# Optimization experiments

Measured on AMD Instinct MI355X. Metric: run time of the kernel, lower is better.

## Reference

```python
import jax, jax.numpy as jnp
import numpy as np

MARGIN = 0.1
NUM_BINS = 1600  # FastAP histogram bins over squared-distance range [0, 4]


def _fastap_rewards(x, labels):
    """Per-query FastAP (Cakir et al.) with soft (triangular) histogram binning.
    x: [n, d] L2-normalized embeddings; labels: [n] int. Returns [n] rewards.
    Uses the fact that a triangular pulse of width delta spreads each distance
    over exactly two adjacent bins -> scatter-add instead of an [n,n,L] tensor."""
    n = x.shape[0]
    L = NUM_BINS + 1
    delta = 4.0 / NUM_BINS
    dist2 = jnp.clip(2.0 - 2.0 * (x @ x.T), 0.0, 4.0)  # [n, n]
    same = labels[:, None] == labels[None, :]
    eye = jnp.eye(n, dtype=bool)
    i_pos = same & ~eye
    i_neg = ~same

    t = dist2 / delta
    idx0 = jnp.clip(jnp.floor(t).astype(jnp.int32), 0, L - 1)
    idx1 = jnp.clip(idx0 + 1, 0, L - 1)
    frac = t - jnp.floor(t)
    rows = jnp.broadcast_to(jnp.arange(n)[:, None], (n, n))

    def hist(mask):
        m = mask.astype(x.dtype)
        h = jnp.zeros((n, L), x.dtype)
        h = h.at[rows, idx0].add((1.0 - frac) * m)
        h = h.at[rows, idx1].add(frac * m)
        return h

    h_pos = hist(i_pos)
    h_neg = hist(i_neg)
    H_pos = jnp.cumsum(h_pos, axis=1)
    H_all = jnp.cumsum(h_pos + h_neg, axis=1)
    n_pos = jnp.sum(i_pos, axis=1).astype(x.dtype)
    safe = H_all > 0
    ap = jnp.sum(jnp.where(safe, h_pos * H_pos / jnp.where(safe, H_all, 1.0), 0.0), axis=1)
    return jnp.where(n_pos > 0, ap / jnp.maximum(n_pos, 1.0), 0.0)


def _per_row_loss(inputs_col, targets_col, inputs_row, targets_row):
    """Vectorized form of compute_loss_list. Sorting in the original only serves
    to extract max pos / max neg similarity, so per-row maxima + masked sums
    reproduce the exact same math."""
    n = inputs_col.shape[0]
    sim = inputs_col @ inputs_row.T  # [n, m]
    pos = targets_col[:, None] == targets_row[None, :]
    neg = ~pos  # computed BEFORE removing the diagonal, as in the original
    eye = jnp.eye(n, dtype=bool)
    pos = pos.at[:, :n].set(pos[:, :n] & ~eye)

    has_pos = jnp.any(pos, axis=1)
    neg_max = jnp.max(jnp.where(neg, sim, -jnp.inf), axis=1)  # neg_pair_[-1]
    pos_max = jnp.max(jnp.where(pos, sim, -jnp.inf), axis=1)  # pos_pair_[-1]

    pos_sel = pos & (sim < (neg_max + MARGIN)[:, None])
    pos_loss = jnp.sum(jnp.where(pos_sel, 1.0 - sim, 0.0), axis=1)

    thr = jnp.maximum(0.6, pos_max) - MARGIN
    neg_sel = neg & (sim > thr[:, None])
    neg_loss = jnp.sum(jnp.where(neg_sel, sim, 0.0), axis=1)

    return jnp.where(has_pos, pos_loss + neg_loss, 0.0), n


def setup_inputs() -> dict:
    key = jax.random.key(0)
    k1, k2, k3, k4, k5 = jax.random.split(key, 5)
    n, m, d, ncls = 4096, 4096, 128, 512

    def unit(k, shape):
        v = jax.random.normal(k, shape, dtype=jnp.float32)
        return v / jnp.linalg.norm(v, axis=-1, keepdims=True)

    return {
        "inputs_col": unit(k1, (n, d)),
        "targets_col": jax.random.randint(k2, (n,), 0, ncls),
        "inputs_row": unit(k3, (m, d)),
        "targets_row": jax.random.randint(k4, (m,), 0, ncls),
        "reward_labels": jax.random.randint(k5, (n,), 0, ncls),
    }


def reference(inputs_col, targets_col, inputs_row, targets_row, reward_labels):
    loss_i, n = _per_row_loss(inputs_col, targets_col, inputs_row, targets_row)
    # torch.tensor(rewards) detaches rewards from the graph -> stop_gradient
    rewards = jax.lax.stop_gradient(_fastap_rewards(inputs_col, reward_labels))
    return jnp.sum(loss_i * (1.0 - rewards)) / n
```

## Files before the change

kernel.cpp:

```cpp
#include <hip/hip_runtime.h>


#define N_ROWS 4096
#define DIM 128
#define TILE 128
#define L_BINS 1601

typedef __bf16 bf16x8 __attribute__((ext_vector_type(8)));
typedef float f32x4 __attribute__((ext_vector_type(4)));

__device__ __forceinline__ unsigned short f32_to_bf16(float f) {
    unsigned int u = __float_as_uint(f);
    u = (u + 0x7FFFu + ((u >> 16) & 1u)) >> 16;
    return (unsigned short)u;
}

__device__ __forceinline__ float bf16_lo(unsigned int u) {
    return __uint_as_float(u << 16);
}
__device__ __forceinline__ float bf16_hi(unsigned int u) {
    return __uint_as_float(u & 0xFFFF0000u);
}

__device__ __forceinline__ void unpack8(uint4 pk, float* s) {
    s[0] = bf16_lo(pk.x); s[1] = bf16_hi(pk.x);
    s[2] = bf16_lo(pk.y); s[3] = bf16_hi(pk.y);
    s[4] = bf16_lo(pk.z); s[5] = bf16_hi(pk.z);
    s[6] = bf16_lo(pk.w); s[7] = bf16_hi(pk.w);
}

__device__ __forceinline__ void async_copy16(const void* g, void* l) {
    __builtin_amdgcn_global_load_lds(
        (const __attribute__((address_space(1))) unsigned int*)g,
        (__attribute__((address_space(3))) unsigned int*)l, 16, 0, 0);
}

__global__ __launch_bounds__(256) void cvt2_kernel(const float4* __restrict__ a,
                                                   const float4* __restrict__ b,
                                                   ushort4* __restrict__ oa,
                                                   ushort4* __restrict__ ob,
                                                   int nvec) {
    for (int idx = blockIdx.x * 256 + threadIdx.x; idx < 2 * nvec; idx += gridDim.x * 256) {
        bool second = idx >= nvec;
        int k = second ? idx - nvec : idx;
        float4 v = second ? b[k] : a[k];
        ushort4 o;
        o.x = f32_to_bf16(v.x); o.y = f32_to_bf16(v.y);
        o.z = f32_to_bf16(v.z); o.w = f32_to_bf16(v.w);
        if (second) ob[k] = o; else oa[k] = o;
    }
}

__global__ __launch_bounds__(256) void gemm_tile_kernel(const unsigned short* __restrict__ A,
                                                        const unsigned short* __restrict__ B0,
                                                        const unsigned short* __restrict__ B1,
                                                        unsigned short* __restrict__ C0,
                                                        unsigned short* __restrict__ C1,
                                                        int N) {
    __shared__ unsigned short As[TILE * DIM];
    __shared__ unsigned short Bs[TILE * DIM];
    int w = threadIdx.x >> 6;
    int lane = threadIdx.x & 63;
    int tm = blockIdx.y, tn = blockIdx.x;
    const unsigned short* B = blockIdx.z ? B1 : B0;
    unsigned short* C = blockIdx.z ? C1 : C0;

    const char* ga = (const char*)(A + (size_t)tm * TILE * DIM);
    const char* gb = (const char*)(B + (size_t)tn * TILE * DIM);
#pragma unroll
    for (int it = 0; it < 8; ++it) {
        int off = (w * 8 + it) * 1024;
        async_copy16(ga + off + lane * 16, (char*)As + off);
        async_copy16(gb + off + lane * 16, (char*)Bs + off);
    }
    __syncthreads();

    int wm = (w & 1) * 64;
    int wn = (w >> 1) * 64;
    int quad = lane >> 4;
    int l15 = lane & 15;

    f32x4 acc[4][4] = {};
#pragma unroll
    for (int kk = 0; kk < 4; ++kk) {
        int kb = kk * 32 + quad * 8;
        bf16x8 af[4], bfr[4];
#pragma unroll
        for (int mi = 0; mi < 4; ++mi)
            af[mi] = *(const bf16x8*)&As[(wm + mi * 16 + l15) * DIM + kb];
#pragma unroll
        for (int ni = 0; ni < 4; ++ni)
            bfr[ni] = *(const bf16x8*)&Bs[(wn + ni * 16 + l15) * DIM + kb];
#pragma unroll
        for (int mi = 0; mi < 4; ++mi)
#pragma unroll
            for (int ni = 0; ni < 4; ++ni)
                acc[mi][ni] = __builtin_amdgcn_mfma_f32_16x16x32_bf16(af[mi], bfr[ni], acc[mi][ni], 0, 0, 0);
    }

#pragma unroll
    for (int mi = 0; mi < 4; ++mi) {
        int row0 = tm * TILE + wm + mi * 16 + quad * 4;
#pragma unroll
        for (int ni = 0; ni < 4; ++ni) {
            int col = tn * TILE + wn + ni * 16 + l15;
#pragma unroll
            for (int r = 0; r < 4; ++r)
                C[(size_t)(row0 + r) * N + col] = f32_to_bf16(acc[mi][ni][r]);
        }
    }
}

__global__ __launch_bounds__(256) void loss_kernel(const unsigned short* __restrict__ sim,
                                                   const int* __restrict__ tcol,
                                                   const int* __restrict__ trow,
                                                   float* __restrict__ loss,
                                                   int n, int m) {
    int i = (blockIdx.x * 256 + threadIdx.x) >> 6;
    int lane = threadIdx.x & 63;
    int myt = tcol[i];

    const uint4* simv = (const uint4*)(sim + (size_t)i * m);
    const int4* labv = (const int4*)trow;

    uint4 pk[8];
    unsigned long long posm = 0ull, negm = 0ull;
    float pmax = -3e38f, nmax = -3e38f;
#pragma unroll
    for (int v = 0; v < 8; ++v) {
        int vi = v * 64 + lane;
        pk[v] = simv[vi];
        int4 l0 = labv[2 * vi];
        int4 l1 = labv[2 * vi + 1];
        int j0 = vi * 8;
        float s[8];
        unpack8(pk[v], s);
        int lab[8] = {l0.x, l0.y, l0.z, l0.w, l1.x, l1.y, l1.z, l1.w};
#pragma unroll
        for (int k = 0; k < 8; ++k) {
            int j = j0 + k;
            bool same = (lab[k] == myt);
            bool posf = same && (j != i);
            if (posf) pmax = fmaxf(pmax, s[k]);
            if (!same) nmax = fmaxf(nmax, s[k]);
            posm |= ((unsigned long long)posf) << (v * 8 + k);
            negm |= ((unsigned long long)(!same)) << (v * 8 + k);
        }
    }
#pragma unroll
    for (int off = 32; off > 0; off >>= 1) {
        pmax = fmaxf(pmax, __shfl_xor(pmax, off));
        nmax = fmaxf(nmax, __shfl_xor(nmax, off));
    }

    float thr_n = nmax + 0.1f;
    float thr_p = fmaxf(0.6f, pmax) - 0.1f;
    float pl = 0.f, nl = 0.f;
#pragma unroll
    for (int v = 0; v < 8; ++v) {
        float s[8];
        unpack8(pk[v], s);
#pragma unroll
        for (int k = 0; k < 8; ++k) {
            int bit = v * 8 + k;
            bool posf = (posm >> bit) & 1ull;
            bool negf = (negm >> bit) & 1ull;
            pl += (posf && s[k] < thr_n) ? 1.f - s[k] : 0.f;
            nl += (negf && s[k] > thr_p) ? s[k] : 0.f;
        }
    }
    float tot = pl + nl;
#pragma unroll
    for (int off = 32; off > 0; off >>= 1) tot += __shfl_xor(tot, off);
    if (lane == 0) loss[i] = (pmax > -1e30f) ? tot : 0.f;
}

__global__ __launch_bounds__(256) void fastap_kernel(const unsigned short* __restrict__ gram,
                                                     const int* __restrict__ labels,
                                                     float* __restrict__ reward,
                                                     int n) {
    __shared__ unsigned long long hist[L_BINS];
    __shared__ unsigned long long wsum[4];
    __shared__ float apw[4];
    __shared__ int npw[4];
    int i = blockIdx.x;
    int t = threadIdx.x;
    int w = t >> 6;
    int lane = t & 63;

    for (int b = t; b < L_BINS; b += 256) hist[b] = 0ull;
    __syncthreads();

    int li = labels[i];
    int npos = 0;
    const uint4* gv = (const uint4*)(gram + (size_t)i * n);
    const int4* labv = (const int4*)labels;

    for (int v = t; v < (n >> 3); v += 256) {
        uint4 pk = gv[v];
        int4 l0 = labv[2 * v];
        int4 l1 = labv[2 * v + 1];
        int j0 = v << 3;
        float s[8];
        unpack8(pk, s);
        int lab[8] = {l0.x, l0.y, l0.z, l0.w, l1.x, l1.y, l1.z, l1.w};
#pragma unroll
        for (int k = 0; k < 8; ++k) {
            int j = j0 + k;
            float d2 = fminf(fmaxf(2.f - 2.f * s[k], 0.f), 4.f);
            float tt = d2 * 400.0f;
            float fl = floorf(tt);
            int i0 = (int)fl;
            if (i0 > L_BINS - 1) i0 = L_BINS - 1;
            int i1 = i0 + 1;
            if (i1 > L_BINS - 1) i1 = L_BINS - 1;
            unsigned int w1 = (unsigned int)((tt - fl) * 65536.0f);
            unsigned int w0 = 65536u - w1;
            bool diag = (j == i);
            if (diag) { w0 = 0u; w1 = 0u; }
            bool posf = (lab[k] == li) && !diag;
            unsigned long long hi = posf ? 1ull : 0ull;
            atomicAdd(&hist[i0], (unsigned long long)w0 | ((hi * w0) << 32));
            atomicAdd(&hist[i1], (unsigned long long)w1 | ((hi * w1) << 32));
            npos += posf ? 1 : 0;
        }
    }
    __syncthreads();

    const int CH = 7;
    int base = t * CH;
    unsigned long long lc[CH];
    unsigned long long run = 0ull;
#pragma unroll
    for (int k = 0; k < CH; ++k) {
        int idx = base + k;
        unsigned long long h = (idx < L_BINS) ? hist[idx] : 0ull;
        run += h;
        lc[k] = run;
    }
    unsigned long long tsum = run;
    unsigned long long sc = tsum;
#pragma unroll
    for (int off = 1; off < 64; off <<= 1) {
        unsigned long long v2 = __shfl_up(sc, off);
        if (lane >= off) sc += v2;
    }
    if (lane == 63) wsum[w] = sc;
    __syncthreads();
    unsigned long long woff = 0ull;
    for (int ww = 0; ww < w; ++ww) woff += wsum[ww];
    unsigned long long throff = woff + sc - tsum;

    float ap = 0.f;
#pragma unroll
    for (int k = 0; k < CH; ++k) {
        int idx = base + k;
        if (idx < L_BINS) {
            unsigned long long h = hist[idx];
            unsigned int hp = (unsigned int)(h >> 32);
            if (hp) {
                unsigned long long cum = lc[k] + throff;
                unsigned int Hp = (unsigned int)(cum >> 32);
                unsigned int Ha = (unsigned int)cum;
                ap += (float)hp * (float)Hp / (float)Ha;
            }
        }
    }
#pragma unroll
    for (int off = 32; off > 0; off >>= 1) {
        ap += __shfl_xor(ap, off);
        npos += __shfl_xor(npos, off);
    }
    if (lane == 0) { apw[w] = ap; npw[w] = npos; }
    __syncthreads();
    if (t == 0) {
        float A = apw[0] + apw[1] + apw[2] + apw[3];
        int np = npw[0] + npw[1] + npw[2] + npw[3];
        reward[i] = (np > 0) ? A * (1.0f / 65536.0f) / (float)np : 0.f;
    }
}

__global__ __launch_bounds__(256) void final_kernel(const float* __restrict__ loss,
                                                    const float* __restrict__ reward,
                                                    float* __restrict__ out, int n) {
    __shared__ float r[256];
    int t = threadIdx.x;
    float s = 0.f;
    for (int j = t; j < n; j += 256) s += loss[j] * (1.f - reward[j]);
    r[t] = s;
    __syncthreads();
    for (int off = 128; off > 0; off >>= 1) {
        if (t < off) r[t] += r[t + off];
        __syncthreads();
    }
    if (t == 0) out[0] = r[0] / (float)n;
}

extern "C" void kernel_launch(void* const* d_in, const int* in_sizes, int n_in,
                              void* d_out, int out_size, void* d_ws, size_t ws_size,
                              hipStream_t stream) {
    const float* inputs_col = (const float*)d_in[0];
    const int* targets_col = (const int*)d_in[1];
    const float* inputs_row = (const float*)d_in[2];
    const int* targets_row = (const int*)d_in[3];
    const int* reward_labels = (const int*)d_in[4];
    float* out = (float*)d_out;

    const int n = N_ROWS, m = N_ROWS, d = DIM;
    char* ws = (char*)d_ws;
    const size_t MB = 1048576;
    unsigned short* simbuf = (unsigned short*)ws;
    unsigned short* grambuf = (unsigned short*)(ws + 32 * MB);
    unsigned short* Abf = (unsigned short*)(ws + 64 * MB);
    unsigned short* Rbf = (unsigned short*)(ws + 65 * MB);
    float* loss = (float*)(ws + 66 * MB);
    float* reward = loss + n;

    cvt2_kernel<<<512, 256, 0, stream>>>((const float4*)inputs_col, (const float4*)inputs_row,
                                         (ushort4*)Abf, (ushort4*)Rbf, n * d / 4);

    dim3 ggrid(n / TILE, n / TILE, 2);
    gemm_tile_kernel<<<ggrid, 256, 0, stream>>>(Abf, Rbf, Abf, simbuf, grambuf, m);

    loss_kernel<<<n / 4, 256, 0, stream>>>(simbuf, targets_col, targets_row, loss, n, m);

    fastap_kernel<<<n, 256, 0, stream>>>(grambuf, reward_labels, reward, n);

    final_kernel<<<1, 256, 0, stream>>>(loss, reward, out, n);
}
```

Baseline: 135.8 us.

## Fuse bf16 conversion into GEMM and merge loss, FastAP and final reduction

Drops the separate fp32-to-bf16 conversion kernel. The GEMM now loads fp32 inputs directly, packs them to bf16 and stores them into LDS, in place of the async global-to-LDS copy. The loss, FastAP and final-reduction kernels are merged into one tail kernel, whose last-finishing block (tracked by an atomic counter) computes the final sum. This removes three launches and the intermediate bf16 buffers, at the cost of a memset, more global load traffic in the GEMM (fp32, re-read per tile), and synchronous register-staged LDS fills.

```diff
diff --git a/kernel.cpp b/kernel.cpp
--- a/kernel.cpp
+++ b/kernel.cpp
@@ -14,13 +14,11 @@
     u = (u + 0x7FFFu + ((u >> 16) & 1u)) >> 16;
     return (unsigned short)u;
 }
-
-__device__ __forceinline__ float bf16_lo(unsigned int u) {
-    return __uint_as_float(u << 16);
-}
-__device__ __forceinline__ float bf16_hi(unsigned int u) {
-    return __uint_as_float(u & 0xFFFF0000u);
-}
+__device__ __forceinline__ unsigned int pack2(float x, float y) {
+    return (unsigned int)f32_to_bf16(x) | ((unsigned int)f32_to_bf16(y) << 16);
+}
+__device__ __forceinline__ float bf16_lo(unsigned int u) { return __uint_as_float(u << 16); }
+__device__ __forceinline__ float bf16_hi(unsigned int u) { return __uint_as_float(u & 0xFFFF0000u); }
 
 __device__ __forceinline__ void unpack8(uint4 pk, float* s) {
     s[0] = bf16_lo(pk.x); s[1] = bf16_hi(pk.x);
@@ -29,49 +27,32 @@
     s[6] = bf16_lo(pk.w); s[7] = bf16_hi(pk.w);
 }
 
-__device__ __forceinline__ void async_copy16(const void* g, void* l) {
-    __builtin_amdgcn_global_load_lds(
-        (const __attribute__((address_space(1))) unsigned int*)g,
-        (__attribute__((address_space(3))) unsigned int*)l, 16, 0, 0);
-}
-
-__global__ __launch_bounds__(256) void cvt2_kernel(const float4* __restrict__ a,
-                                                   const float4* __restrict__ b,
-                                                   ushort4* __restrict__ oa,
-                                                   ushort4* __restrict__ ob,
-                                                   int nvec) {
-    for (int idx = blockIdx.x * 256 + threadIdx.x; idx < 2 * nvec; idx += gridDim.x * 256) {
-        bool second = idx >= nvec;
-        int k = second ? idx - nvec : idx;
-        float4 v = second ? b[k] : a[k];
-        ushort4 o;
-        o.x = f32_to_bf16(v.x); o.y = f32_to_bf16(v.y);
-        o.z = f32_to_bf16(v.z); o.w = f32_to_bf16(v.w);
-        if (second) ob[k] = o; else oa[k] = o;
-    }
-}
-
-__global__ __launch_bounds__(256) void gemm_tile_kernel(const unsigned short* __restrict__ A,
-                                                        const unsigned short* __restrict__ B0,
-                                                        const unsigned short* __restrict__ B1,
-                                                        unsigned short* __restrict__ C0,
-                                                        unsigned short* __restrict__ C1,
-                                                        int N) {
-    __shared__ unsigned short As[TILE * DIM];
-    __shared__ unsigned short Bs[TILE * DIM];
-    int w = threadIdx.x >> 6;
-    int lane = threadIdx.x & 63;
+__global__ __launch_bounds__(256) void gemm_kernel(
+    const float* __restrict__ incol, const float* __restrict__ inrow,
+    unsigned short* __restrict__ simbuf, unsigned short* __restrict__ grambuf) {
+    __shared__ __align__(16) unsigned short As[TILE * DIM];
+    __shared__ __align__(16) unsigned short Bs[TILE * DIM];
+    int t = threadIdx.x;
+    int w = t >> 6, lane = t & 63;
     int tm = blockIdx.y, tn = blockIdx.x;
-    const unsigned short* B = blockIdx.z ? B1 : B0;
-    unsigned short* C = blockIdx.z ? C1 : C0;
-
-    const char* ga = (const char*)(A + (size_t)tm * TILE * DIM);
-    const char* gb = (const char*)(B + (size_t)tn * TILE * DIM);
+    const float* ga = incol + (size_t)tm * TILE * DIM;
+    const float* gb = (blockIdx.z ? incol : inrow) + (size_t)tn * TILE * DIM;
+    unsigned short* C = blockIdx.z ? grambuf : simbuf;
+
 #pragma unroll
     for (int it = 0; it < 8; ++it) {
-        int off = (w * 8 + it) * 1024;
-        async_copy16(ga + off + lane * 16, (char*)As + off);
-        async_copy16(gb + off + lane * 16, (char*)Bs + off);
+        int fo = it * 2048 + t * 8;
+        float4 a0 = *(const float4*)(ga + fo);
+        float4 a1 = *(const float4*)(ga + fo + 4);
+        float4 b0 = *(const float4*)(gb + fo);
+        float4 b1 = *(const float4*)(gb + fo + 4);
+        uint4 pa, pb;
+        pa.x = pack2(a0.x, a0.y); pa.y = pack2(a0.z, a0.w);
+        pa.z = pack2(a1.x, a1.y); pa.w = pack2(a1.z, a1.w);
+        pb.x = pack2(b0.x, b0.y); pb.y = pack2(b0.z, b0.w);
+        pb.z = pack2(b1.x, b1.y); pb.w = pack2(b1.z, b1.w);
+        *(uint4*)((char*)As + it * 4096 + t * 16) = pa;
+        *(uint4*)((char*)Bs + it * 4096 + t * 16) = pb;
     }
     __syncthreads();
 
@@ -79,7 +60,6 @@
     int wn = (w >> 1) * 64;
     int quad = lane >> 4;
     int l15 = lane & 15;
-
     f32x4 acc[4][4] = {};
 #pragma unroll
     for (int kk = 0; kk < 4; ++kk) {
@@ -97,7 +77,6 @@
             for (int ni = 0; ni < 4; ++ni)
                 acc[mi][ni] = __builtin_amdgcn_mfma_f32_16x16x32_bf16(af[mi], bfr[ni], acc[mi][ni], 0, 0, 0);
     }
-
 #pragma unroll
     for (int mi = 0; mi < 4; ++mi) {
         int row0 = tm * TILE + wm + mi * 16 + quad * 4;
@@ -106,194 +85,185 @@
             int col = tn * TILE + wn + ni * 16 + l15;
 #pragma unroll
             for (int r = 0; r < 4; ++r)
-                C[(size_t)(row0 + r) * N + col] = f32_to_bf16(acc[mi][ni][r]);
-        }
-    }
-}
-
-__global__ __launch_bounds__(256) void loss_kernel(const unsigned short* __restrict__ sim,
-                                                   const int* __restrict__ tcol,
-                                                   const int* __restrict__ trow,
-                                                   float* __restrict__ loss,
-                                                   int n, int m) {
-    int i = (blockIdx.x * 256 + threadIdx.x) >> 6;
-    int lane = threadIdx.x & 63;
-    int myt = tcol[i];
-
-    const uint4* simv = (const uint4*)(sim + (size_t)i * m);
-    const int4* labv = (const int4*)trow;
-
-    uint4 pk[8];
-    unsigned long long posm = 0ull, negm = 0ull;
-    float pmax = -3e38f, nmax = -3e38f;
-#pragma unroll
-    for (int v = 0; v < 8; ++v) {
-        int vi = v * 64 + lane;
-        pk[v] = simv[vi];
-        int4 l0 = labv[2 * vi];
-        int4 l1 = labv[2 * vi + 1];
-        int j0 = vi * 8;
-        float s[8];
-        unpack8(pk[v], s);
-        int lab[8] = {l0.x, l0.y, l0.z, l0.w, l1.x, l1.y, l1.z, l1.w};
-#pragma unroll
-        for (int k = 0; k < 8; ++k) {
-            int j = j0 + k;
-            bool same = (lab[k] == myt);
-            bool posf = same && (j != i);
-            if (posf) pmax = fmaxf(pmax, s[k]);
-            if (!same) nmax = fmaxf(nmax, s[k]);
-            posm |= ((unsigned long long)posf) << (v * 8 + k);
-            negm |= ((unsigned long long)(!same)) << (v * 8 + k);
-        }
-    }
-#pragma unroll
-    for (int off = 32; off > 0; off >>= 1) {
-        pmax = fmaxf(pmax, __shfl_xor(pmax, off));
-        nmax = fmaxf(nmax, __shfl_xor(nmax, off));
-    }
-
-    float thr_n = nmax + 0.1f;
-    float thr_p = fmaxf(0.6f, pmax) - 0.1f;
-    float pl = 0.f, nl = 0.f;
-#pragma unroll
-    for (int v = 0; v < 8; ++v) {
-        float s[8];
-        unpack8(pk[v], s);
-#pragma unroll
-        for (int k = 0; k < 8; ++k) {
-            int bit = v * 8 + k;
-            bool posf = (posm >> bit) & 1ull;
-            bool negf = (negm >> bit) & 1ull;
-            pl += (posf && s[k] < thr_n) ? 1.f - s[k] : 0.f;
-            nl += (negf && s[k] > thr_p) ? s[k] : 0.f;
-        }
-    }
-    float tot = pl + nl;
-#pragma unroll
-    for (int off = 32; off > 0; off >>= 1) tot += __shfl_xor(tot, off);
-    if (lane == 0) loss[i] = (pmax > -1e30f) ? tot : 0.f;
-}
-
-__global__ __launch_bounds__(256) void fastap_kernel(const unsigned short* __restrict__ gram,
-                                                     const int* __restrict__ labels,
-                                                     float* __restrict__ reward,
-                                                     int n) {
+                C[(size_t)(row0 + r) * N_ROWS + col] = f32_to_bf16(acc[mi][ni][r]);
+        }
+    }
+}
+
+__global__ __launch_bounds__(256) void tail_kernel(
+    const unsigned short* __restrict__ simbuf, const unsigned short* __restrict__ grambuf,
+    const int* __restrict__ tcol, const int* __restrict__ trow, const int* __restrict__ rlab,
+    float* __restrict__ lossv, float* __restrict__ rewardv,
+    unsigned int* __restrict__ counter, float* __restrict__ out) {
     __shared__ unsigned long long hist[L_BINS];
-    __shared__ unsigned long long wsum[4];
-    __shared__ float apw[4];
-    __shared__ int npw[4];
-    int i = blockIdx.x;
+    __shared__ unsigned long long wsumA[4];
+    __shared__ float apwA[4];
+    __shared__ int npwA[4];
+    __shared__ unsigned int sdone;
+    int b = blockIdx.x;
     int t = threadIdx.x;
-    int w = t >> 6;
-    int lane = t & 63;
-
-    for (int b = t; b < L_BINS; b += 256) hist[b] = 0ull;
+    int w = t >> 6, lane = t & 63;
+
+    if (b < 1024) {
+        int i = b * 4 + w;
+        int myt = tcol[i];
+        const uint4* simv = (const uint4*)(simbuf + (size_t)i * N_ROWS);
+        const int4* labv = (const int4*)trow;
+        uint4 pk[8];
+        unsigned long long posm = 0ull, negm = 0ull;
+        float pmax = -3e38f, nmax = -3e38f;
+#pragma unroll
+        for (int v = 0; v < 8; ++v) {
+            int vi = v * 64 + lane;
+            pk[v] = simv[vi];
+            int4 l0 = labv[2 * vi];
+            int4 l1 = labv[2 * vi + 1];
+            int j0 = vi * 8;
+            float s[8];
+            unpack8(pk[v], s);
+            int lab[8] = {l0.x, l0.y, l0.z, l0.w, l1.x, l1.y, l1.z, l1.w};
+#pragma unroll
+            for (int k = 0; k < 8; ++k) {
+                int j = j0 + k;
+                bool same = (lab[k] == myt);
+                bool posf = same && (j != i);
+                if (posf) pmax = fmaxf(pmax, s[k]);
+                if (!same) nmax = fmaxf(nmax, s[k]);
+                posm |= ((unsigned long long)posf) << (v * 8 + k);
+                negm |= ((unsigned long long)(!same)) << (v * 8 + k);
+            }
+        }
+#pragma unroll
+        for (int off = 32; off > 0; off >>= 1) {
+            pmax = fmaxf(pmax, __shfl_xor(pmax, off));
+            nmax = fmaxf(nmax, __shfl_xor(nmax, off));
+        }
+        float thr_n = nmax + 0.1f;
+        float thr_p = fmaxf(0.6f, pmax) - 0.1f;
+        float pl = 0.f, nl = 0.f;
+#pragma unroll
+        for (int v = 0; v < 8; ++v) {
+            float s[8];
+            unpack8(pk[v], s);
+#pragma unroll
+            for (int k = 0; k < 8; ++k) {
+                int bit = v * 8 + k;
+                pl += (((posm >> bit) & 1ull) && s[k] < thr_n) ? 1.f - s[k] : 0.f;
+                nl += (((negm >> bit) & 1ull) && s[k] > thr_p) ? s[k] : 0.f;
+            }
+        }
+        float tot = pl + nl;
+#pragma unroll
+        for (int off = 32; off > 0; off >>= 1) tot += __shfl_xor(tot, off);
+        if (lane == 0) lossv[i] = (pmax > -1e30f) ? tot : 0.f;
+    } else {
+        int i = b - 1024;
+        for (int bb = t; bb < L_BINS; bb += 256) hist[bb] = 0ull;
+        __syncthreads();
+        int li = rlab[i];
+        int npos = 0;
+        const uint4* gv = (const uint4*)(grambuf + (size_t)i * N_ROWS);
+        const int4* labv = (const int4*)rlab;
+        for (int v = t; v < (N_ROWS >> 3); v += 256) {
+            uint4 pk = gv[v];
+            int4 l0 = labv[2 * v];
+            int4 l1 = labv[2 * v + 1];
+            int j0 = v << 3;
+            float s[8];
+            unpack8(pk, s);
+            int lab[8] = {l0.x, l0.y, l0.z, l0.w, l1.x, l1.y, l1.z, l1.w};
+#pragma unroll
+            for (int k = 0; k < 8; ++k) {
+                int j = j0 + k;
+                float d2 = fminf(fmaxf(2.f - 2.f * s[k], 0.f), 4.f);
+                float tt = d2 * 400.0f;
+                float fl = floorf(tt);
+                int i0 = (int)fl;
+                if (i0 > L_BINS - 1) i0 = L_BINS - 1;
+                int i1 = i0 + 1;
+                if (i1 > L_BINS - 1) i1 = L_BINS - 1;
+                unsigned int w1 = (unsigned int)((tt - fl) * 65536.0f);
+                unsigned int w0 = 65536u - w1;
+                bool diag = (j == i);
+                if (diag) { w0 = 0u; w1 = 0u; }
+                bool posf = (lab[k] == li) && !diag;
+                unsigned long long hi = posf ? 1ull : 0ull;
+                atomicAdd(&hist[i0], (unsigned long long)w0 | ((hi * w0) << 32));
+                atomicAdd(&hist[i1], (unsigned long long)w1 | ((hi * w1) << 32));
+                npos += posf ? 1 : 0;
+            }
+        }
+        __syncthreads();
+
+        const int CH = 7;
+        int base = t * CH;
+        unsigned long long lc[CH];
+        unsigned long long run = 0ull;
+#pragma unroll
+        for (int k = 0; k < CH; ++k) {
+            int idx = base + k;
+            unsigned long long h = (idx < L_BINS) ? hist[idx] : 0ull;
+            run += h;
+            lc[k] = run;
+        }
+        unsigned long long tsum = run;
+        unsigned long long sc = tsum;
+#pragma unroll
+        for (int off = 1; off < 64; off <<= 1) {
+            unsigned long long v2 = __shfl_up(sc, off);
+            if (lane >= off) sc += v2;
+        }
+        if (lane == 63) wsumA[w] = sc;
+        __syncthreads();
+        unsigned long long woff = 0ull;
+        for (int ww = 0; ww < w; ++ww) woff += wsumA[ww];
+        unsigned long long throff = woff + sc - tsum;
+
+        float ap = 0.f;
+#pragma unroll
+        for (int k = 0; k < CH; ++k) {
+            int idx = base + k;
+            if (idx < L_BINS) {
+                unsigned long long h = hist[idx];
+                unsigned int hp = (unsigned int)(h >> 32);
+                if (hp) {
+                    unsigned long long cum = lc[k] + throff;
+                    ap += (float)hp * (float)(unsigned int)(cum >> 32) / (float)(unsigned int)cum;
+                }
+            }
+        }
+#pragma unroll
+        for (int off = 32; off > 0; off >>= 1) {
+            ap += __shfl_xor(ap, off);
+            npos += __shfl_xor(npos, off);
+        }
+        if (lane == 0) { apwA[w] = ap; npwA[w] = npos; }
+        __syncthreads();
+        if (t == 0) {
+            float A = apwA[0] + apwA[1] + apwA[2] + apwA[3];
+            int np = npwA[0] + npwA[1] + npwA[2] + npwA[3];
+            rewardv[i] = (np > 0) ? A * (1.0f / 65536.0f) / (float)np : 0.f;
+        }
+    }
+
+    __threadfence();
     __syncthreads();
-
-    int li = labels[i];
-    int npos = 0;
-    const uint4* gv = (const uint4*)(gram + (size_t)i * n);
-    const int4* labv = (const int4*)labels;
-
-    for (int v = t; v < (n >> 3); v += 256) {
-        uint4 pk = gv[v];
-        int4 l0 = labv[2 * v];
-        int4 l1 = labv[2 * v + 1];
-        int j0 = v << 3;
-        float s[8];
-        unpack8(pk, s);
-        int lab[8] = {l0.x, l0.y, l0.z, l0.w, l1.x, l1.y, l1.z, l1.w};
-#pragma unroll
-        for (int k = 0; k < 8; ++k) {
-            int j = j0 + k;
-            float d2 = fminf(fmaxf(2.f - 2.f * s[k], 0.f), 4.f);
-            float tt = d2 * 400.0f;
-            float fl = floorf(tt);
-            int i0 = (int)fl;
-            if (i0 > L_BINS - 1) i0 = L_BINS - 1;
-            int i1 = i0 + 1;
-            if (i1 > L_BINS - 1) i1 = L_BINS - 1;
-            unsigned int w1 = (unsigned int)((tt - fl) * 65536.0f);
-            unsigned int w0 = 65536u - w1;
-            bool diag = (j == i);
-            if (diag) { w0 = 0u; w1 = 0u; }
-            bool posf = (lab[k] == li) && !diag;
-            unsigned long long hi = posf ? 1ull : 0ull;
-            atomicAdd(&hist[i0], (unsigned long long)w0 | ((hi * w0) << 32));
-            atomicAdd(&hist[i1], (unsigned long long)w1 | ((hi * w1) << 32));
-            npos += posf ? 1 : 0;
-        }
-    }
+    if (t == 0) sdone = atomicAdd(counter, 1u);
     __syncthreads();
-
-    const int CH = 7;
-    int base = t * CH;
-    unsigned long long lc[CH];
-    unsigned long long run = 0ull;
-#pragma unroll
-    for (int k = 0; k < CH; ++k) {
-        int idx = base + k;
-        unsigned long long h = (idx < L_BINS) ? hist[idx] : 0ull;
-        run += h;
-        lc[k] = run;
-    }
-    unsigned long long tsum = run;
-    unsigned long long sc = tsum;
-#pragma unroll
-    for (int off = 1; off < 64; off <<= 1) {
-        unsigned long long v2 = __shfl_up(sc, off);
-        if (lane >= off) sc += v2;
-    }
-    if (lane == 63) wsum[w] = sc;
-    __syncthreads();
-    unsigned long long woff = 0ull;
-    for (int ww = 0; ww < w; ++ww) woff += wsum[ww];
-    unsigned long long throff = woff + sc - tsum;
-
-    float ap = 0.f;
-#pragma unroll
-    for (int k = 0; k < CH; ++k) {
-        int idx = base + k;
-        if (idx < L_BINS) {
-            unsigned long long h = hist[idx];
-            unsigned int hp = (unsigned int)(h >> 32);
-            if (hp) {
-                unsigned long long cum = lc[k] + throff;
-                unsigned int Hp = (unsigned int)(cum >> 32);
-                unsigned int Ha = (unsigned int)cum;
-                ap += (float)hp * (float)Hp / (float)Ha;
-            }
-        }
-    }
-#pragma unroll
-    for (int off = 32; off > 0; off >>= 1) {
-        ap += __shfl_xor(ap, off);
-        npos += __shfl_xor(npos, off);
-    }
-    if (lane == 0) { apw[w] = ap; npw[w] = npos; }
-    __syncthreads();
-    if (t == 0) {
-        float A = apw[0] + apw[1] + apw[2] + apw[3];
-        int np = npw[0] + npw[1] + npw[2] + npw[3];
-        reward[i] = (np > 0) ? A * (1.0f / 65536.0f) / (float)np : 0.f;
-    }
-}
-
-__global__ __launch_bounds__(256) void final_kernel(const float* __restrict__ loss,
-                                                    const float* __restrict__ reward,
-                                                    float* __restrict__ out, int n) {
-    __shared__ float r[256];
-    int t = threadIdx.x;
-    float s = 0.f;
-    for (int j = t; j < n; j += 256) s += loss[j] * (1.f - reward[j]);
-    r[t] = s;
-    __syncthreads();
-    for (int off = 128; off > 0; off >>= 1) {
-        if (t < off) r[t] += r[t + off];
-        __syncthreads();
-    }
-    if (t == 0) out[0] = r[0] / (float)n;
+    if (sdone == gridDim.x - 1) {
+        __threadfence();
+        float s = 0.f;
+        for (int j = t; j < N_ROWS; j += 256) {
+            float lv = __hip_atomic_load(&lossv[j], __ATOMIC_RELAXED, __HIP_MEMORY_SCOPE_AGENT);
+            float rv = __hip_atomic_load(&rewardv[j], __ATOMIC_RELAXED, __HIP_MEMORY_SCOPE_AGENT);
+            s += lv * (1.f - rv);
+        }
+#pragma unroll
+        for (int off = 32; off > 0; off >>= 1) s += __shfl_xor(s, off);
+        if (lane == 0) apwA[w] = s;
+        __syncthreads();
+        if (t == 0) out[0] = (apwA[0] + apwA[1] + apwA[2] + apwA[3]) / (float)N_ROWS;
+    }
 }
 
 extern "C" void kernel_launch(void* const* d_in, const int* in_sizes, int n_in,
@@ -306,25 +276,20 @@
     const int* reward_labels = (const int*)d_in[4];
     float* out = (float*)d_out;
 
-    const int n = N_ROWS, m = N_ROWS, d = DIM;
     char* ws = (char*)d_ws;
     const size_t MB = 1048576;
     unsigned short* simbuf = (unsigned short*)ws;
     unsigned short* grambuf = (unsigned short*)(ws + 32 * MB);
-    unsigned short* Abf = (unsigned short*)(ws + 64 * MB);
-    unsigned short* Rbf = (unsigned short*)(ws + 65 * MB);
-    float* loss = (float*)(ws + 66 * MB);
-    float* reward = loss + n;
-
-    cvt2_kernel<<<512, 256, 0, stream>>>((const float4*)inputs_col, (const float4*)inputs_row,
-                                         (ushort4*)Abf, (ushort4*)Rbf, n * d / 4);
-
-    dim3 ggrid(n / TILE, n / TILE, 2);
-    gemm_tile_kernel<<<ggrid, 256, 0, stream>>>(Abf, Rbf, Abf, simbuf, grambuf, m);
-
-    loss_kernel<<<n / 4, 256, 0, stream>>>(simbuf, targets_col, targets_row, loss, n, m);
-
-    fastap_kernel<<<n, 256, 0, stream>>>(grambuf, reward_labels, reward, n);
-
-    final_kernel<<<1, 256, 0, stream>>>(loss, reward, out, n);
-}
+    float* lossv = (float*)(ws + 64 * MB);
+    float* rewardv = (float*)(ws + 64 * MB + 16384);
+    unsigned int* counter = (unsigned int*)(ws + 64 * MB + 32768);
+
+    hipMemsetAsync(counter, 0, 4, stream);
+
+    dim3 ggrid(N_ROWS / TILE, N_ROWS / TILE, 2);
+    gemm_kernel<<<ggrid, 256, 0, stream>>>(inputs_col, inputs_row, simbuf, grambuf);
+
+    tail_kernel<<<1024 + N_ROWS, 256, 0, stream>>>(simbuf, grambuf,
+                                                   targets_col, targets_row, reward_labels,
+                                                   lossv, rewardv, counter, out);
+}
```

After: 516.3 us. +280.3%, slower.
